# Performance work log

Measured on AMD Instinct MI355X. Metric: run time of the kernel, lower is better.

Reference implementation:

```python
import math
import jax, jax.numpy as jnp
import numpy as np

D_MODEL = 1024
D_HIDDEN = 2048
N_EXPERTS = 8
TOP_K = 2
CAPACITY_FACTOR = 1.25


def setup_inputs() -> dict:
    key = jax.random.key(0)
    k0, k1, k2, k3 = jax.random.split(key, 4)
    B, T = 2, 2048
    x = jax.random.normal(k0, (B, T, D_MODEL), dtype=jnp.float32)
    # torch nn.Linear stores weight as [out_features, in_features]
    w_router = jax.random.normal(k1, (N_EXPERTS, D_MODEL), dtype=jnp.float32) * 0.02
    w_gate = jax.random.normal(k2, (D_HIDDEN, D_MODEL), dtype=jnp.float32) * 0.02
    w_down = jax.random.normal(k3, (N_EXPERTS, D_MODEL, D_HIDDEN), dtype=jnp.float32) * 0.02
    return {"x": x, "w_router": w_router, "w_gate": w_gate, "w_down": w_down}


def _moe_forward(x, w_router, w_gate, w_down):
    B, T, D = x.shape
    N = B * T
    xf = x.reshape(N, D)

    # Router (computed in fp32, as in the original)
    logits = xf.astype(jnp.float32) @ w_router.T            # [N, E]
    gates = jax.nn.softmax(logits, axis=-1)                  # [N, E]
    topk_gates, topk_idx = jax.lax.top_k(gates, TOP_K)       # [N, K]

    # expert_mask[n, e] = 1 if expert e is among token n's top-k
    expert_mask = jax.nn.one_hot(topk_idx, N_EXPERTS, dtype=jnp.int32).sum(axis=1)  # [N, E]

    # Capacity masking via cumulative position within each expert's buffer
    capacity = math.ceil(N / N_EXPERTS * CAPACITY_FACTOR)
    position_in_expert = jnp.cumsum(expert_mask, axis=0) - 1
    expert_mask = expert_mask * (position_in_expert < capacity)

    keep = jnp.take_along_axis(expert_mask, topk_idx, axis=1) > 0  # [N, K]
    topk_gates = topk_gates * keep
    topk_gates = topk_gates / (topk_gates.sum(axis=-1, keepdims=True) + 1e-6)

    # Shared up-projection + SiLU (dropout = 0)
    hidden = jax.nn.silu(xf @ w_gate.T)                      # [N, H]

    # combine[n, e] = sum_k topk_gates[n, k] * [topk_idx[n, k] == e]
    combine = (topk_gates[:, :, None]
               * jax.nn.one_hot(topk_idx, N_EXPERTS, dtype=topk_gates.dtype)).sum(axis=1)  # [N, E]

    # Combine: y[n] = sum_e combine[n, e] * (hidden[n] @ w_down[e].T)
    # (dropped tokens have combine weight 0, matching the gated index_add in torch)
    y = jnp.zeros((N, D), dtype=x.dtype)
    for e in range(N_EXPERTS):  # small fixed loop over experts
        y = y + combine[:, e:e + 1] * (hidden @ w_down[e].T)
    return y.reshape(B, T, D)


def reference(x, w_router, w_gate, w_down):
    return _moe_forward(x, w_router, w_gate, w_down)
```

## Files before the change

kernel.cpp:

```cpp
#include <hip/hip_runtime.h>
#include <hip/hip_bf16.h>
#include <math.h>

#define NTOK 4096
#define DMODEL 1024
#define DHID 2048
#define NEXP 8
#define CAP 640
#define SLOTS (NEXP * CAP)

typedef __attribute__((ext_vector_type(8))) short short8;
typedef __attribute__((ext_vector_type(4))) float f32x4;

__device__ inline short f2bf(float f) {
    union { float f; unsigned u; } v; v.f = f;
    unsigned r = v.u + 0x7FFF + ((v.u >> 16) & 1);
    return (short)(r >> 16);
}
__device__ inline float bf2f(unsigned short u) {
    union { unsigned u; float f; } v; v.u = ((unsigned)u) << 16; return v.f;
}
__device__ inline void async16(const short* g, short* l) {
    __builtin_amdgcn_global_load_lds(
        (const __attribute__((address_space(1))) unsigned*)g,
        (__attribute__((address_space(3))) unsigned*)l, 16, 0, 0);
}

__global__ __launch_bounds__(256) void router_kernel(
        const float* __restrict__ x, const float* __restrict__ wr, short* __restrict__ Xb,
        int2* __restrict__ topk_idx, float2* __restrict__ topk_gate)
{
    const int token = blockIdx.x * 4 + (threadIdx.x >> 6);
    const int lane  = threadIdx.x & 63;
    const float* xr = x + (size_t)token * DMODEL + lane * 16;
    float4 xv[4];
#pragma unroll
    for (int j = 0; j < 4; j++) xv[j] = ((const float4*)xr)[j];
    short8 s0 = { f2bf(xv[0].x), f2bf(xv[0].y), f2bf(xv[0].z), f2bf(xv[0].w),
                  f2bf(xv[1].x), f2bf(xv[1].y), f2bf(xv[1].z), f2bf(xv[1].w) };
    short8 s1 = { f2bf(xv[2].x), f2bf(xv[2].y), f2bf(xv[2].z), f2bf(xv[2].w),
                  f2bf(xv[3].x), f2bf(xv[3].y), f2bf(xv[3].z), f2bf(xv[3].w) };
    short* xo = Xb + (size_t)token * DMODEL + lane * 16;
    *(short8*)xo = s0;
    *(short8*)(xo + 8) = s1;

    float acc[NEXP];
#pragma unroll
    for (int e = 0; e < NEXP; e++) acc[e] = 0.f;
#pragma unroll
    for (int j = 0; j < 4; j++) {
#pragma unroll
        for (int e = 0; e < NEXP; e++) {
            float4 wv = ((const float4*)(wr + e * DMODEL + lane * 16))[j];
            acc[e] += xv[j].x * wv.x + xv[j].y * wv.y + xv[j].z * wv.z + xv[j].w * wv.w;
        }
    }
#pragma unroll
    for (int off = 32; off >= 1; off >>= 1) {
#pragma unroll
        for (int e = 0; e < NEXP; e++) acc[e] += __shfl_xor(acc[e], off, 64);
    }
    if (lane == 0) {
        float m = acc[0];
#pragma unroll
        for (int e = 1; e < NEXP; e++) m = fmaxf(m, acc[e]);
        float den = 0.f, g[NEXP];
#pragma unroll
        for (int e = 0; e < NEXP; e++) { g[e] = __expf(acc[e] - m); den += g[e]; }
        float inv = 1.f / den;
#pragma unroll
        for (int e = 0; e < NEXP; e++) g[e] *= inv;
        int i0 = 0; float l0 = acc[0];
#pragma unroll
        for (int e = 1; e < NEXP; e++) if (acc[e] > l0) { l0 = acc[e]; i0 = e; }
        int i1 = -1; float l1 = -1e30f;
#pragma unroll
        for (int e = 0; e < NEXP; e++) if (e != i0 && acc[e] > l1) { l1 = acc[e]; i1 = e; }
        topk_idx[token]  = make_int2(i0, i1);
        topk_gate[token] = make_float2(g[i0], g[i1]);
    }
}

__global__ __launch_bounds__(256) void router_fb_kernel(
        const float* __restrict__ x, const float* __restrict__ wr,
        int2* __restrict__ topk_idx, float2* __restrict__ topk_gate)
{
    const int token = blockIdx.x * 4 + (threadIdx.x >> 6);
    const int lane  = threadIdx.x & 63;
    const float* xr = x + (size_t)token * DMODEL + lane * 16;
    float acc[NEXP];
#pragma unroll
    for (int e = 0; e < NEXP; e++) acc[e] = 0.f;
#pragma unroll
    for (int j = 0; j < 4; j++) {
        float4 xv = ((const float4*)xr)[j];
#pragma unroll
        for (int e = 0; e < NEXP; e++) {
            float4 wv = ((const float4*)(wr + e * DMODEL + lane * 16))[j];
            acc[e] += xv.x * wv.x + xv.y * wv.y + xv.z * wv.z + xv.w * wv.w;
        }
    }
#pragma unroll
    for (int off = 32; off >= 1; off >>= 1) {
#pragma unroll
        for (int e = 0; e < NEXP; e++) acc[e] += __shfl_xor(acc[e], off, 64);
    }
    if (lane == 0) {
        float m = acc[0];
#pragma unroll
        for (int e = 1; e < NEXP; e++) m = fmaxf(m, acc[e]);
        float den = 0.f, g[NEXP];
#pragma unroll
        for (int e = 0; e < NEXP; e++) { g[e] = __expf(acc[e] - m); den += g[e]; }
        float inv = 1.f / den;
#pragma unroll
        for (int e = 0; e < NEXP; e++) g[e] *= inv;
        int i0 = 0; float l0 = acc[0];
#pragma unroll
        for (int e = 1; e < NEXP; e++) if (acc[e] > l0) { l0 = acc[e]; i0 = e; }
        int i1 = -1; float l1 = -1e30f;
#pragma unroll
        for (int e = 0; e < NEXP; e++) if (e != i0 && acc[e] > l1) { l1 = acc[e]; i1 = e; }
        topk_idx[token]  = make_int2(i0, i1);
        topk_gate[token] = make_float2(g[i0], g[i1]);
    }
}

__global__ __launch_bounds__(256) void convert2_kernel(
        const float* __restrict__ a, short* __restrict__ da, size_t na,
        const float* __restrict__ b, short* __restrict__ db)
{
    size_t i = ((size_t)blockIdx.x * 256 + threadIdx.x) * 8;
    const float* src; short* dst;
    if (i < na) { src = a + i; dst = da + i; }
    else        { src = b + (i - na); dst = db + (i - na); }
    float4 v0 = ((const float4*)src)[0];
    float4 v1 = ((const float4*)src)[1];
    short8 s = { f2bf(v0.x), f2bf(v0.y), f2bf(v0.z), f2bf(v0.w),
                 f2bf(v1.x), f2bf(v1.y), f2bf(v1.z), f2bf(v1.w) };
    *(short8*)dst = s;
}

__global__ __launch_bounds__(1024) void scan_kernel(
        const int2* __restrict__ topk_idx, const float2* __restrict__ topk_gate,
        int* __restrict__ gtok, float* __restrict__ gw, int* __restrict__ gcnt,
        int2* __restrict__ tslot, float2* __restrict__ tw)
{
    __shared__ unsigned long long wt0[16], wt1[16];
    const int th = threadIdx.x, lane = th & 63, wid = th >> 6;
    int2 idx[4]; float2 gt[4];
#pragma unroll
    for (int j = 0; j < 4; j++) { idx[j] = topk_idx[th * 4 + j]; gt[j] = topk_gate[th * 4 + j]; }
    unsigned long long c0 = 0, c1 = 0;
#pragma unroll
    for (int j = 0; j < 4; j++) {
        int e0 = idx[j].x, e1 = idx[j].y;
        if (e0 < 4) c0 += 1ull << (e0 * 16); else c1 += 1ull << ((e0 - 4) * 16);
        if (e1 < 4) c0 += 1ull << (e1 * 16); else c1 += 1ull << ((e1 - 4) * 16);
    }
    const unsigned long long my0 = c0, my1 = c1;
#pragma unroll
    for (int d = 1; d < 64; d <<= 1) {
        unsigned long long t0 = __shfl_up(c0, d, 64);
        unsigned long long t1 = __shfl_up(c1, d, 64);
        if (lane >= d) { c0 += t0; c1 += t1; }
    }
    if (lane == 63) { wt0[wid] = c0; wt1[wid] = c1; }
    __syncthreads();
    unsigned long long o0 = 0, o1 = 0;
    for (int w = 0; w < wid; w++) { o0 += wt0[w]; o1 += wt1[w]; }
    c0 += o0; c1 += o1;
    if (th == 1023) {
#pragma unroll
        for (int e = 0; e < 4; e++) gcnt[e]     = min((int)((c0 >> (e * 16)) & 0xFFFF), CAP);
#pragma unroll
        for (int e = 0; e < 4; e++) gcnt[4 + e] = min((int)((c1 >> (e * 16)) & 0xFFFF), CAP);
    }
    const unsigned long long x0 = c0 - my0, x1 = c1 - my1;
    int base[NEXP];
#pragma unroll
    for (int e = 0; e < 4; e++) base[e]     = (int)((x0 >> (e * 16)) & 0xFFFF);
#pragma unroll
    for (int e = 0; e < 4; e++) base[4 + e] = (int)((x1 >> (e * 16)) & 0xFFFF);
#pragma unroll
    for (int j = 0; j < 4; j++) {
        const int n = th * 4 + j;
        const int e0 = idx[j].x, e1 = idx[j].y;
        const int p0 = base[e0]++;
        const int p1 = base[e1]++;
        const bool k0 = p0 < CAP, k1 = p1 < CAP;
        const float gg0 = k0 ? gt[j].x : 0.f, gg1 = k1 ? gt[j].y : 0.f;
        const float invs = 1.f / (gg0 + gg1 + 1e-6f);
        const int s0 = k0 ? e0 * CAP + p0 : 0;
        const int s1 = k1 ? e1 * CAP + p1 : 0;
        if (k0) { gtok[s0] = n; gw[s0] = gg0 * invs; }
        if (k1) { gtok[s1] = n; gw[s1] = gg1 * invs; }
        tslot[n] = make_int2(s0, s1);
        tw[n]    = make_float2(gg0 * invs, gg1 * invs);
    }
}

__global__ __launch_bounds__(256) void gemm1_kernel(
        const short* __restrict__ Xb, const short* __restrict__ WGb,
        short* __restrict__ Hid, short* __restrict__ Hp, int KS)
{
    __shared__ __align__(16) short As[128 * 64];
    __shared__ __align__(16) short Bs[128 * 64];
    const int t = threadIdx.x;
    const int wave = t >> 6, lane = t & 63;
    const int m0 = (blockIdx.y / KS) * 128, n0 = blockIdx.x * 128;
    const int ks = blockIdx.y % KS;
    const int wm = (wave >> 1) * 64, wn = (wave & 1) * 64;
    const int lm = lane & 15, lq = lane >> 4;

    const short *ga[4], *gb[4];
    short *la[4], *lb[4];
#pragma unroll
    for (int j = 0; j < 4; j++) {
        const int b   = wave * 4 + j;
        const int row = (b >> 1) * 16 + lm;
        const int col = (b & 1) * 32 + lq * 8;
        la[j] = &As[b * 512 + lane * 8];
        lb[j] = &Bs[b * 512 + lane * 8];
        ga[j] = Xb  + (size_t)(m0 + row) * DMODEL + col;
        gb[j] = WGb + (size_t)(n0 + row) * DMODEL + col;
    }

    f32x4 acc[4][4];
#pragma unroll
    for (int a = 0; a < 4; a++)
#pragma unroll
        for (int b = 0; b < 4; b++) acc[a][b] = (f32x4)(0.f);

    const int kbeg = ks * (DMODEL / KS), kend = kbeg + DMODEL / KS;
    for (int k0 = kbeg; k0 < kend; k0 += 64) {
#pragma unroll
        for (int j = 0; j < 4; j++) { async16(ga[j] + k0, la[j]); async16(gb[j] + k0, lb[j]); }
        __syncthreads();
#pragma unroll
        for (int kk = 0; kk < 2; kk++) {
            short8 af[4], bf[4];
#pragma unroll
            for (int mi = 0; mi < 4; mi++)
                af[mi] = *(const short8*)&As[((((wm >> 4) + mi) * 2 + kk) * 64 + lane) * 8];
#pragma unroll
            for (int ni = 0; ni < 4; ni++)
                bf[ni] = *(const short8*)&Bs[((((wn >> 4) + ni) * 2 + kk) * 64 + lane) * 8];
#pragma unroll
            for (int mi = 0; mi < 4; mi++)
#pragma unroll
                for (int ni = 0; ni < 4; ni++)
                    acc[mi][ni] = __builtin_amdgcn_mfma_f32_16x16x32_bf16(af[mi], bf[ni], acc[mi][ni], 0, 0, 0);
        }
        __syncthreads();
    }
    if (KS == 1) {
#pragma unroll
        for (int mi = 0; mi < 4; mi++)
#pragma unroll
            for (int i = 0; i < 4; i++) {
                const int row = m0 + wm + mi * 16 + lq * 4 + i;
#pragma unroll
                for (int ni = 0; ni < 4; ni++) {
                    const int col = n0 + wn + ni * 16 + lm;
                    const float v = acc[mi][ni][i];
                    Hid[(size_t)row * DHID + col] = f2bf(v / (1.f + __expf(-v)));
                }
            }
    } else {
        short* Ho = Hp + (size_t)ks * NTOK * DHID;
#pragma unroll
        for (int mi = 0; mi < 4; mi++)
#pragma unroll
            for (int i = 0; i < 4; i++) {
                const int row = m0 + wm + mi * 16 + lq * 4 + i;
#pragma unroll
                for (int ni = 0; ni < 4; ni++) {
                    const int col = n0 + wn + ni * 16 + lm;
                    Ho[(size_t)row * DHID + col] = f2bf(acc[mi][ni][i]);
                }
            }
    }
}

__global__ __launch_bounds__(256) void silu_merge_kernel(
        const short* __restrict__ Hp, short* __restrict__ Hid)
{
    const size_t i = ((size_t)blockIdx.x * 256 + threadIdx.x) * 8;
    const unsigned short* p0 = (const unsigned short*)Hp + i;
    const unsigned short* p1 = (const unsigned short*)Hp + (size_t)NTOK * DHID + i;
    ushort4 a0 = *(const ushort4*)p0, a1 = *(const ushort4*)(p0 + 4);
    ushort4 b0 = *(const ushort4*)p1, b1 = *(const ushort4*)(p1 + 4);
    float v[8] = { bf2f(a0.x) + bf2f(b0.x), bf2f(a0.y) + bf2f(b0.y),
                   bf2f(a0.z) + bf2f(b0.z), bf2f(a0.w) + bf2f(b0.w),
                   bf2f(a1.x) + bf2f(b1.x), bf2f(a1.y) + bf2f(b1.y),
                   bf2f(a1.z) + bf2f(b1.z), bf2f(a1.w) + bf2f(b1.w) };
    short8 o;
#pragma unroll
    for (int j = 0; j < 8; j++) o[j] = f2bf(v[j] / (1.f + __expf(-v[j])));
    *(short8*)(Hid + i) = o;
}

__global__ __launch_bounds__(256) void gemm2_kernel(
        const short* __restrict__ Hid, const short* __restrict__ WDb,
        const int* __restrict__ gtok, const int* __restrict__ gcnt,
        short* __restrict__ Yp, int KS)
{
    __shared__ __align__(16) short As[128 * 64];
    __shared__ __align__(16) short Bs[128 * 64];
    __shared__ int tok_s[128];
    const int e  = blockIdx.x;
    const int n0 = blockIdx.y * 128;
    const int m0 = (blockIdx.z / KS) * 128;
    const int ks = blockIdx.z % KS;
    const int cnt = gcnt[e];
    if (m0 >= cnt) return;
    const int t = threadIdx.x;
    const int wave = t >> 6, lane = t & 63;
    const int wm = (wave >> 1) * 64, wn = (wave & 1) * 64;
    const int lm = lane & 15, lq = lane >> 4;
    const short* WDe = WDb + (size_t)e * DMODEL * DHID;

    if (t < 128) tok_s[t] = (m0 + t < cnt) ? gtok[e * CAP + m0 + t] : 0;
    __syncthreads();

    const short *ga[4], *gb[4];
    short *la[4], *lb[4];
#pragma unroll
    for (int j = 0; j < 4; j++) {
        const int b   = wave * 4 + j;
        const int row = (b >> 1) * 16 + lm;
        const int col = (b & 1) * 32 + lq * 8;
        la[j] = &As[b * 512 + lane * 8];
        lb[j] = &Bs[b * 512 + lane * 8];
        ga[j] = Hid + (size_t)tok_s[row] * DHID + col;
        gb[j] = WDe + (size_t)(n0 + row) * DHID + col;
    }

    f32x4 acc[4][4];
#pragma unroll
    for (int a = 0; a < 4; a++)
#pragma unroll
        for (int b = 0; b < 4; b++) acc[a][b] = (f32x4)(0.f);

    const int kbeg = ks * (DHID / KS), kend = kbeg + DHID / KS;
    for (int k0 = kbeg; k0 < kend; k0 += 64) {
#pragma unroll
        for (int j = 0; j < 4; j++) { async16(ga[j] + k0, la[j]); async16(gb[j] + k0, lb[j]); }
        __syncthreads();
#pragma unroll
        for (int kk = 0; kk < 2; kk++) {
            short8 af[4], bf[4];
#pragma unroll
            for (int mi = 0; mi < 4; mi++)
                af[mi] = *(const short8*)&As[((((wm >> 4) + mi) * 2 + kk) * 64 + lane) * 8];
#pragma unroll
            for (int ni = 0; ni < 4; ni++)
                bf[ni] = *(const short8*)&Bs[((((wn >> 4) + ni) * 2 + kk) * 64 + lane) * 8];
#pragma unroll
            for (int mi = 0; mi < 4; mi++)
#pragma unroll
                for (int ni = 0; ni < 4; ni++)
                    acc[mi][ni] = __builtin_amdgcn_mfma_f32_16x16x32_bf16(af[mi], bf[ni], acc[mi][ni], 0, 0, 0);
        }
        __syncthreads();
    }
    short* Yo = Yp + (size_t)ks * SLOTS * DMODEL;
#pragma unroll
    for (int mi = 0; mi < 4; mi++)
#pragma unroll
        for (int i = 0; i < 4; i++) {
            const int slot = e * CAP + m0 + wm + mi * 16 + lq * 4 + i;
#pragma unroll
            for (int ni = 0; ni < 4; ni++) {
                const int col = n0 + wn + ni * 16 + lm;
                Yo[(size_t)slot * DMODEL + col] = f2bf(acc[mi][ni][i]);
            }
        }
}

__global__ __launch_bounds__(256) void combine_kernel(
        const short* __restrict__ Yp, const int2* __restrict__ tslot,
        const float2* __restrict__ tw, float* __restrict__ y, int KS)
{
    const int token = blockIdx.x;
    const int c = threadIdx.x * 4;
    const int2   s = tslot[token];
    const float2 w = tw[token];
    float4 o = make_float4(0.f, 0.f, 0.f, 0.f);
    for (int ks = 0; ks < KS; ks++) {
        const unsigned short* base = (const unsigned short*)Yp + (size_t)ks * SLOTS * DMODEL;
        ushort4 a = *(const ushort4*)(base + (size_t)s.x * DMODEL + c);
        ushort4 b = *(const ushort4*)(base + (size_t)s.y * DMODEL + c);
        o.x += w.x * bf2f(a.x) + w.y * bf2f(b.x);
        o.y += w.x * bf2f(a.y) + w.y * bf2f(b.y);
        o.z += w.x * bf2f(a.z) + w.y * bf2f(b.z);
        o.w += w.x * bf2f(a.w) + w.y * bf2f(b.w);
    }
    *(float4*)&y[(size_t)token * DMODEL + c] = o;
}

__global__ __launch_bounds__(256) void gemm1_fb_kernel(
        const float* __restrict__ X, const float* __restrict__ WG, short* __restrict__ Hid)
{
    __shared__ short As[128][72];
    __shared__ short Bs[128][72];
    const int t = threadIdx.x;
    const int wave = t >> 6, lane = t & 63;
    const int m0 = blockIdx.y * 128, n0 = blockIdx.x * 128;
    const int wm = (wave >> 1) * 64, wn = (wave & 1) * 64;
    const int lm = lane & 15, lq = lane >> 4, lk = lq * 8;
    const int r0 = t >> 3, c8 = (t & 7) * 8;

    f32x4 acc[4][4];
#pragma unroll
    for (int a = 0; a < 4; a++)
#pragma unroll
        for (int b = 0; b < 4; b++) acc[a][b] = (f32x4)(0.f);

    for (int k0 = 0; k0 < DMODEL; k0 += 64) {
#pragma unroll
        for (int i = 0; i < 4; i++) {
            const int row = r0 + i * 32;
            const float* ga = X + (size_t)(m0 + row) * DMODEL + k0 + c8;
            float4 v0 = ((const float4*)ga)[0];
            float4 v1 = ((const float4*)ga)[1];
            short8 s = { f2bf(v0.x), f2bf(v0.y), f2bf(v0.z), f2bf(v0.w),
                         f2bf(v1.x), f2bf(v1.y), f2bf(v1.z), f2bf(v1.w) };
            *(short8*)&As[row][c8] = s;
            const float* gb = WG + (size_t)(n0 + row) * DMODEL + k0 + c8;
            float4 w0 = ((const float4*)gb)[0];
            float4 w1 = ((const float4*)gb)[1];
            short8 sw = { f2bf(w0.x), f2bf(w0.y), f2bf(w0.z), f2bf(w0.w),
                          f2bf(w1.x), f2bf(w1.y), f2bf(w1.z), f2bf(w1.w) };
            *(short8*)&Bs[row][c8] = sw;
        }
        __syncthreads();
#pragma unroll
        for (int kk = 0; kk < 64; kk += 32) {
            short8 af[4], bf[4];
#pragma unroll
            for (int mi = 0; mi < 4; mi++) af[mi] = *(const short8*)&As[wm + mi * 16 + lm][kk + lk];
#pragma unroll
            for (int ni = 0; ni < 4; ni++) bf[ni] = *(const short8*)&Bs[wn + ni * 16 + lm][kk + lk];
#pragma unroll
            for (int mi = 0; mi < 4; mi++)
#pragma unroll
                for (int ni = 0; ni < 4; ni++)
                    acc[mi][ni] = __builtin_amdgcn_mfma_f32_16x16x32_bf16(af[mi], bf[ni], acc[mi][ni], 0, 0, 0);
        }
        __syncthreads();
    }
#pragma unroll
    for (int mi = 0; mi < 4; mi++)
#pragma unroll
        for (int i = 0; i < 4; i++) {
            const int row = m0 + wm + mi * 16 + lq * 4 + i;
#pragma unroll
            for (int ni = 0; ni < 4; ni++) {
                const int col = n0 + wn + ni * 16 + lm;
                const float v = acc[mi][ni][i];
                const float s = v / (1.f + __expf(-v));
                Hid[(size_t)row * DHID + col] = f2bf(s);
            }
        }
}

__global__ __launch_bounds__(256) void gemm2_fb_kernel(
        const short* __restrict__ Hid, const float* __restrict__ WD,
        const int* __restrict__ gtok, const float* __restrict__ gw,
        const int* __restrict__ gcnt, float* __restrict__ Y)
{
    __shared__ short As[128][72];
    __shared__ short Bs[128][72];
    __shared__ int   tok_s[128];
    __shared__ float w_s[128];
    const int e = blockIdx.z;
    const int cnt = gcnt[e];
    const int m0 = blockIdx.y * 128;
    if (m0 >= cnt) return;
    const int n0 = blockIdx.x * 128;
    const int t = threadIdx.x;
    const int wave = t >> 6, lane = t & 63;
    const int wm = (wave >> 1) * 64, wn = (wave & 1) * 64;
    const int lm = lane & 15, lq = lane >> 4, lk = lq * 8;
    const int r0 = t >> 3, c8 = (t & 7) * 8;
    const float* WDe = WD + (size_t)e * DMODEL * DHID;

    if (t < 128) {
        const int r = m0 + t;
        const bool v = r < cnt;
        tok_s[t] = v ? gtok[e * CAP + r] : 0;
        w_s[t]   = v ? gw[e * CAP + r] : 0.f;
    }
    __syncthreads();

    f32x4 acc[4][4];
#pragma unroll
    for (int a = 0; a < 4; a++)
#pragma unroll
        for (int b = 0; b < 4; b++) acc[a][b] = (f32x4)(0.f);

    const int tokA[4] = { tok_s[r0], tok_s[r0 + 32], tok_s[r0 + 64], tok_s[r0 + 96] };

    for (int k0 = 0; k0 < DHID; k0 += 64) {
#pragma unroll
        for (int i = 0; i < 4; i++) {
            const int row = r0 + i * 32;
            uint4 av = *(const uint4*)(Hid + (size_t)tokA[i] * DHID + k0 + c8);
            *(uint4*)&As[row][c8] = av;
            const float* gb = WDe + (size_t)(n0 + row) * DHID + k0 + c8;
            float4 w0 = ((const float4*)gb)[0];
            float4 w1 = ((const float4*)gb)[1];
            short8 sw = { f2bf(w0.x), f2bf(w0.y), f2bf(w0.z), f2bf(w0.w),
                          f2bf(w1.x), f2bf(w1.y), f2bf(w1.z), f2bf(w1.w) };
            *(short8*)&Bs[row][c8] = sw;
        }
        __syncthreads();
#pragma unroll
        for (int kk = 0; kk < 64; kk += 32) {
            short8 af[4], bf[4];
#pragma unroll
            for (int mi = 0; mi < 4; mi++) af[mi] = *(const short8*)&As[wm + mi * 16 + lm][kk + lk];
#pragma unroll
            for (int ni = 0; ni < 4; ni++) bf[ni] = *(const short8*)&Bs[wn + ni * 16 + lm][kk + lk];
#pragma unroll
            for (int mi = 0; mi < 4; mi++)
#pragma unroll
                for (int ni = 0; ni < 4; ni++)
                    acc[mi][ni] = __builtin_amdgcn_mfma_f32_16x16x32_bf16(af[mi], bf[ni], acc[mi][ni], 0, 0, 0);
        }
        __syncthreads();
    }
#pragma unroll
    for (int mi = 0; mi < 4; mi++)
#pragma unroll
        for (int i = 0; i < 4; i++) {
            const int r = wm + mi * 16 + lq * 4 + i;
            const float wr = w_s[r];
            if (wr > 0.f) {
                const int token = tok_s[r];
#pragma unroll
                for (int ni = 0; ni < 4; ni++) {
                    const int col = n0 + wn + ni * 16 + lm;
                    atomicAdd(&Y[(size_t)token * DMODEL + col], acc[mi][ni][i] * wr);
                }
            }
        }
}

extern "C" void kernel_launch(void* const* d_in, const int* in_sizes, int n_in,
                              void* d_out, int out_size, void* d_ws, size_t ws_size,
                              hipStream_t stream) {
    const float* x  = (const float*)d_in[0];
    const float* wr = (const float*)d_in[1];
    const float* wg = (const float*)d_in[2];
    const float* wd = (const float*)d_in[3];
    float* y = (float*)d_out;

    char* w = (char*)d_ws;
    int2*   topk_idx  = (int2*)w;    w += NTOK * sizeof(int2);
    float2* topk_gate = (float2*)w;  w += NTOK * sizeof(float2);
    int*    gtok      = (int*)w;     w += NEXP * CAP * sizeof(int);
    float*  gw        = (float*)w;   w += NEXP * CAP * sizeof(float);
    int*    gcnt      = (int*)w;     w += 256;
    int2*   tslot     = (int2*)w;    w += NTOK * sizeof(int2);
    float2* tw        = (float2*)w;  w += NTOK * sizeof(float2);
    short*  Hid       = (short*)w;   w += (size_t)NTOK * DHID * sizeof(short);
    short*  WDb       = (short*)w;   w += (size_t)NEXP * DMODEL * DHID * sizeof(short);
    short*  Xb        = (short*)w;
    short*  WGb       = (short*)(w + (size_t)NTOK * DMODEL * sizeof(short));
    short*  Yp        = (short*)w;
    char*   w63       = w + ((size_t)NTOK * DMODEL + (size_t)DHID * DMODEL) * sizeof(short);
    short*  Hp        = (short*)w63;
    char*   w96       = w63 + (size_t)2 * NTOK * DHID * sizeof(short);
    const size_t need63 = (size_t)(w63 - (char*)d_ws);
    const size_t need96 = (size_t)(w96 - (char*)d_ws);

    if (ws_size >= need63) {
        const int KS1 = (ws_size >= need96) ? 2 : 1;
        const int KS2 = (ws_size >= need96) ? 4 : 1;
        router_kernel<<<NTOK / 4, 256, 0, stream>>>(x, wr, Xb, topk_idx, topk_gate);
        convert2_kernel<<<(DHID * DMODEL + NEXP * DMODEL * DHID) / (256 * 8), 256, 0, stream>>>(
            wg, WGb, (size_t)DHID * DMODEL, wd, WDb);
        scan_kernel<<<1, 1024, 0, stream>>>(topk_idx, topk_gate, gtok, gw, gcnt, tslot, tw);
        gemm1_kernel<<<dim3(DHID / 128, (NTOK / 128) * KS1), 256, 0, stream>>>(
            Xb, WGb, Hid, Hp, KS1);
        if (KS1 == 2)
            silu_merge_kernel<<<(NTOK * DHID) / (256 * 8), 256, 0, stream>>>(Hp, Hid);
        gemm2_kernel<<<dim3(NEXP, DMODEL / 128, (CAP / 128) * KS2), 256, 0, stream>>>(
            Hid, WDb, gtok, gcnt, Yp, KS2);
        combine_kernel<<<NTOK, 256, 0, stream>>>(Yp, tslot, tw, y, KS2);
    } else {
        hipMemsetAsync(y, 0, (size_t)NTOK * DMODEL * sizeof(float), stream);
        router_fb_kernel<<<NTOK / 4, 256, 0, stream>>>(x, wr, topk_idx, topk_gate);
        scan_kernel<<<1, 1024, 0, stream>>>(topk_idx, topk_gate, gtok, gw, gcnt, tslot, tw);
        gemm1_fb_kernel<<<dim3(DHID / 128, NTOK / 128), 256, 0, stream>>>(x, wg, Hid);
        gemm2_fb_kernel<<<dim3(DMODEL / 128, (CAP + 127) / 128, NEXP), 256, 0, stream>>>(
            Hid, wd, gtok, gw, gcnt, y);
    }
}
```

Before: 249.1 us.

## Fuse router with weight conversion and drop split-K in up-projection GEMM

Merges the router/x-conversion kernel and the fp32-to-bf16 weight conversion kernel into a single prep kernel, so one launch covers both. Removes the split-K path for the first GEMM along with its silu_merge kernel, so SiLU is always applied in the GEMM epilogue with no partial-sum buffer round trip. This saves two launches and the Hp write/read traffic, at the cost of fewer blocks for gemm1 (512 tiles). Workspace sizing is also recomputed because Hp no longer exists.

```diff
diff --git a/kernel.cpp b/kernel.cpp
--- a/kernel.cpp
+++ b/kernel.cpp
@@ -8,6 +8,8 @@
 #define NEXP 8
 #define CAP 640
 #define SLOTS (NEXP * CAP)
+#define NWG ((size_t)DHID * DMODEL)
+#define NWD ((size_t)NEXP * DMODEL * DHID)
 
 typedef __attribute__((ext_vector_type(8))) short short8;
 typedef __attribute__((ext_vector_type(4))) float f32x4;
@@ -26,10 +28,24 @@
         (__attribute__((address_space(3))) unsigned*)l, 16, 0, 0);
 }
 
-__global__ __launch_bounds__(256) void router_kernel(
+__global__ __launch_bounds__(256) void prep_kernel(
         const float* __restrict__ x, const float* __restrict__ wr, short* __restrict__ Xb,
-        int2* __restrict__ topk_idx, float2* __restrict__ topk_gate)
-{
+        int2* __restrict__ topk_idx, float2* __restrict__ topk_gate,
+        const float* __restrict__ wg, short* __restrict__ WGb,
+        const float* __restrict__ wd, short* __restrict__ WDb)
+{
+    {
+        const size_t ci = ((size_t)blockIdx.x * 256 + threadIdx.x) * 8;
+        const float* src; short* dst;
+        if (ci < NWG) { src = wg + ci; dst = WGb + ci; }
+        else          { src = wd + (ci - NWG); dst = WDb + (ci - NWG); }
+        float4 v0 = ((const float4*)src)[0];
+        float4 v1 = ((const float4*)src)[1];
+        short8 s = { f2bf(v0.x), f2bf(v0.y), f2bf(v0.z), f2bf(v0.w),
+                     f2bf(v1.x), f2bf(v1.y), f2bf(v1.z), f2bf(v1.w) };
+        *(short8*)dst = s;
+    }
+    if (blockIdx.x >= NTOK / 4) return;
     const int token = blockIdx.x * 4 + (threadIdx.x >> 6);
     const int lane  = threadIdx.x & 63;
     const float* xr = x + (size_t)token * DMODEL + lane * 16;
@@ -124,21 +140,6 @@
         topk_idx[token]  = make_int2(i0, i1);
         topk_gate[token] = make_float2(g[i0], g[i1]);
     }
-}
-
-__global__ __launch_bounds__(256) void convert2_kernel(
-        const float* __restrict__ a, short* __restrict__ da, size_t na,
-        const float* __restrict__ b, short* __restrict__ db)
-{
-    size_t i = ((size_t)blockIdx.x * 256 + threadIdx.x) * 8;
-    const float* src; short* dst;
-    if (i < na) { src = a + i; dst = da + i; }
-    else        { src = b + (i - na); dst = db + (i - na); }
-    float4 v0 = ((const float4*)src)[0];
-    float4 v1 = ((const float4*)src)[1];
-    short8 s = { f2bf(v0.x), f2bf(v0.y), f2bf(v0.z), f2bf(v0.w),
-                 f2bf(v1.x), f2bf(v1.y), f2bf(v1.z), f2bf(v1.w) };
-    *(short8*)dst = s;
 }
 
 __global__ __launch_bounds__(1024) void scan_kernel(
@@ -201,15 +202,13 @@
 }
 
 __global__ __launch_bounds__(256) void gemm1_kernel(
-        const short* __restrict__ Xb, const short* __restrict__ WGb,
-        short* __restrict__ Hid, short* __restrict__ Hp, int KS)
+        const short* __restrict__ Xb, const short* __restrict__ WGb, short* __restrict__ Hid)
 {
     __shared__ __align__(16) short As[128 * 64];
     __shared__ __align__(16) short Bs[128 * 64];
     const int t = threadIdx.x;
     const int wave = t >> 6, lane = t & 63;
-    const int m0 = (blockIdx.y / KS) * 128, n0 = blockIdx.x * 128;
-    const int ks = blockIdx.y % KS;
+    const int m0 = blockIdx.y * 128, n0 = blockIdx.x * 128;
     const int wm = (wave >> 1) * 64, wn = (wave & 1) * 64;
     const int lm = lane & 15, lq = lane >> 4;
 
@@ -232,8 +231,7 @@
 #pragma unroll
         for (int b = 0; b < 4; b++) acc[a][b] = (f32x4)(0.f);
 
-    const int kbeg = ks * (DMODEL / KS), kend = kbeg + DMODEL / KS;
-    for (int k0 = kbeg; k0 < kend; k0 += 64) {
+    for (int k0 = 0; k0 < DMODEL; k0 += 64) {
 #pragma unroll
         for (int j = 0; j < 4; j++) { async16(ga[j] + k0, la[j]); async16(gb[j] + k0, lb[j]); }
         __syncthreads();
@@ -254,51 +252,18 @@
         }
         __syncthreads();
     }
-    if (KS == 1) {
-#pragma unroll
-        for (int mi = 0; mi < 4; mi++)
-#pragma unroll
-            for (int i = 0; i < 4; i++) {
-                const int row = m0 + wm + mi * 16 + lq * 4 + i;
-#pragma unroll
-                for (int ni = 0; ni < 4; ni++) {
-                    const int col = n0 + wn + ni * 16 + lm;
-                    const float v = acc[mi][ni][i];
-                    Hid[(size_t)row * DHID + col] = f2bf(v / (1.f + __expf(-v)));
-                }
+#pragma unroll
+    for (int mi = 0; mi < 4; mi++)
+#pragma unroll
+        for (int i = 0; i < 4; i++) {
+            const int row = m0 + wm + mi * 16 + lq * 4 + i;
+#pragma unroll
+            for (int ni = 0; ni < 4; ni++) {
+                const int col = n0 + wn + ni * 16 + lm;
+                const float v = acc[mi][ni][i];
+                Hid[(size_t)row * DHID + col] = f2bf(v / (1.f + __expf(-v)));
             }
-    } else {
-        short* Ho = Hp + (size_t)ks * NTOK * DHID;
-#pragma unroll
-        for (int mi = 0; mi < 4; mi++)
-#pragma unroll
-            for (int i = 0; i < 4; i++) {
-                const int row = m0 + wm + mi * 16 + lq * 4 + i;
-#pragma unroll
-                for (int ni = 0; ni < 4; ni++) {
-                    const int col = n0 + wn + ni * 16 + lm;
-                    Ho[(size_t)row * DHID + col] = f2bf(acc[mi][ni][i]);
-                }
-            }
-    }
-}
-
-__global__ __launch_bounds__(256) void silu_merge_kernel(
-        const short* __restrict__ Hp, short* __restrict__ Hid)
-{
-    const size_t i = ((size_t)blockIdx.x * 256 + threadIdx.x) * 8;
-    const unsigned short* p0 = (const unsigned short*)Hp + i;
-    const unsigned short* p1 = (const unsigned short*)Hp + (size_t)NTOK * DHID + i;
-    ushort4 a0 = *(const ushort4*)p0, a1 = *(const ushort4*)(p0 + 4);
-    ushort4 b0 = *(const ushort4*)p1, b1 = *(const ushort4*)(p1 + 4);
-    float v[8] = { bf2f(a0.x) + bf2f(b0.x), bf2f(a0.y) + bf2f(b0.y),
-                   bf2f(a0.z) + bf2f(b0.z), bf2f(a0.w) + bf2f(b0.w),
-                   bf2f(a1.x) + bf2f(b1.x), bf2f(a1.y) + bf2f(b1.y),
-                   bf2f(a1.z) + bf2f(b1.z), bf2f(a1.w) + bf2f(b1.w) };
-    short8 o;
-#pragma unroll
-    for (int j = 0; j < 8; j++) o[j] = f2bf(v[j] / (1.f + __expf(-v[j])));
-    *(short8*)(Hid + i) = o;
+        }
 }
 
 __global__ __launch_bounds__(256) void gemm2_kernel(
@@ -571,23 +536,16 @@
     short*  Xb        = (short*)w;
     short*  WGb       = (short*)(w + (size_t)NTOK * DMODEL * sizeof(short));
     short*  Yp        = (short*)w;
-    char*   w63       = w + ((size_t)NTOK * DMODEL + (size_t)DHID * DMODEL) * sizeof(short);
-    short*  Hp        = (short*)w63;
-    char*   w96       = w63 + (size_t)2 * NTOK * DHID * sizeof(short);
-    const size_t need63 = (size_t)(w63 - (char*)d_ws);
-    const size_t need96 = (size_t)(w96 - (char*)d_ws);
+    const size_t span12 = ((size_t)NTOK * DMODEL + (size_t)DHID * DMODEL) * sizeof(short);
+    const size_t need63 = (size_t)(w - (char*)d_ws) + span12;
+    const size_t need96 = (size_t)(w - (char*)d_ws) + (size_t)4 * SLOTS * DMODEL * 2;
 
     if (ws_size >= need63) {
-        const int KS1 = (ws_size >= need96) ? 2 : 1;
         const int KS2 = (ws_size >= need96) ? 4 : 1;
-        router_kernel<<<NTOK / 4, 256, 0, stream>>>(x, wr, Xb, topk_idx, topk_gate);
-        convert2_kernel<<<(DHID * DMODEL + NEXP * DMODEL * DHID) / (256 * 8), 256, 0, stream>>>(
-            wg, WGb, (size_t)DHID * DMODEL, wd, WDb);
+        prep_kernel<<<(int)((NWG + NWD) / 2048), 256, 0, stream>>>(
+            x, wr, Xb, topk_idx, topk_gate, wg, WGb, wd, WDb);
         scan_kernel<<<1, 1024, 0, stream>>>(topk_idx, topk_gate, gtok, gw, gcnt, tslot, tw);
-        gemm1_kernel<<<dim3(DHID / 128, (NTOK / 128) * KS1), 256, 0, stream>>>(
-            Xb, WGb, Hid, Hp, KS1);
-        if (KS1 == 2)
-            silu_merge_kernel<<<(NTOK * DHID) / (256 * 8), 256, 0, stream>>>(Hp, Hid);
+        gemm1_kernel<<<dim3(DHID / 128, NTOK / 128), 256, 0, stream>>>(Xb, WGb, Hid);
         gemm2_kernel<<<dim3(NEXP, DMODEL / 128, (CAP / 128) * KS2), 256, 0, stream>>>(
             Hid, WDb, gtok, gcnt, Yp, KS2);
         combine_kernel<<<NTOK, 256, 0, stream>>>(Yp, tslot, tw, y, KS2);
```

New measurement: 238.5 us. 4.2% less time.
